# Kernel tuning notes

Measured on AMD Instinct MI355X. Metric: run time of the kernel, lower is better.

## Reference

```python
import jax, jax.numpy as jnp
import numpy as np

DIM = 2048
NH = 16
HD = DIM // NH  # 128


def setup_inputs() -> dict:
    key = jax.random.key(0)
    ks = jax.random.split(key, 9)
    s_in = 1.0 / np.sqrt(DIM)
    inp = {
        "x": jax.random.normal(ks[0], (2, 2048, DIM), dtype=jnp.float32),
        # torch Linear weights stored as (out, in); we keep (in, out) for x @ W
        "wq": jax.random.uniform(ks[1], (DIM, DIM), jnp.float32, -s_in, s_in),
        "bq": jax.random.uniform(ks[2], (DIM,), jnp.float32, -s_in, s_in),
        "wk": jax.random.uniform(ks[3], (DIM, HD), jnp.float32, -s_in, s_in),
        "bk": jax.random.uniform(ks[4], (HD,), jnp.float32, -s_in, s_in),
        "wv": jax.random.uniform(ks[5], (DIM, HD), jnp.float32, -s_in, s_in),
        "bv": jax.random.uniform(ks[6], (HD,), jnp.float32, -s_in, s_in),
        "wo": jax.random.uniform(ks[7], (DIM, DIM), jnp.float32, -s_in, s_in),
        "bo": jax.random.uniform(ks[8], (DIM,), jnp.float32, -s_in, s_in),
    }
    return inp


def reference(x, wq, bq, wk, bk, wv, bv, wo, bo):
    bs, sl, dim = x.shape
    q = x @ wq + bq                      # [b, s, dim]
    k = x @ wk + bk                      # [b, s, hd] (single shared KV head)
    v = x @ wv + bv                      # [b, s, hd]
    q = q.reshape(bs, sl, NH, HD)        # [b, s, h, hd]
    scale = 1.0 / np.sqrt(HD).astype(np.float32)
    # scores: broadcast single KV head over all query heads
    attn = jnp.einsum('bshd,btd->bhst', q, k) * scale   # [b, h, s, s]
    att = jax.nn.softmax(attn, axis=-1)
    o = jnp.einsum('bhst,btd->bshd', att, v)            # [b, s, h, hd]
    o = o.reshape(bs, sl, dim)
    return o @ wo + bo
```

## Files before the change

kernel.cpp:

```cpp
#include <hip/hip_runtime.h>
#include <hip/hip_bf16.h>
#include <math.h>

#define DIM 2048
#define NH 16
#define HD 128
#define BATCH 2
#define SEQ 2048
#define TOKENS (BATCH * SEQ)
#define NQKV (DIM + 2 * HD)

typedef __attribute__((ext_vector_type(8))) _Float16 f16x8;
typedef __attribute__((ext_vector_type(4))) float f32x4;
typedef unsigned short u16;
typedef unsigned int u32;

typedef union { u32 d[4]; f16x8 v; } frag_u;

__device__ __forceinline__ u16 f2h(float f) {
    union { _Float16 h; u16 u; } v; v.h = (_Float16)f; return v.u;
}
__device__ __forceinline__ void gll16(const void* g, void* l) {
    __builtin_amdgcn_global_load_lds(
        (const __attribute__((address_space(1))) unsigned int*)g,
        (__attribute__((address_space(3))) unsigned int*)l, 16, 0, 0);
}

__global__ __launch_bounds__(256) void conv_f16(
    const float* __restrict__ in, u16* __restrict__ out)
{
    const int i = blockIdx.x * 256 + threadIdx.x;
    const float4 v = ((const float4*)in)[i];
    ushort4 h;
    h.x = f2h(v.x); h.y = f2h(v.y); h.z = f2h(v.z); h.w = f2h(v.w);
    ((ushort4*)out)[i] = h;
}

__global__ __launch_bounds__(256) void transpose_f16(
    const float* __restrict__ W, u16* __restrict__ T, int K, int N, int rowoff)
{
    __shared__ float tile[32][33];
    const int k0 = blockIdx.x * 32;
    const int n0 = blockIdx.y * 32;
    const int tid = threadIdx.x;
#pragma unroll
    for (int i = 0; i < 4; ++i) {
        const int idx = tid + i * 256;
        const int r = idx >> 5, c = idx & 31;
        tile[r][c] = W[(size_t)(k0 + r) * N + n0 + c];
    }
    __syncthreads();
#pragma unroll
    for (int i = 0; i < 4; ++i) {
        const int idx = tid + i * 256;
        const int r = idx >> 5, c = idx & 31;
        T[(size_t)(rowoff + n0 + r) * K + k0 + c] = f2h(tile[c][r]);
    }
}

__global__ __launch_bounds__(256) void concat_bias(
    const float* __restrict__ bq, const float* __restrict__ bk,
    const float* __restrict__ bv, float* __restrict__ bc)
{
    const int i = blockIdx.x * 256 + threadIdx.x;
    float v;
    if (i < DIM) v = bq[i];
    else if (i < DIM + HD) v = bk[i - DIM];
    else v = bv[i - DIM - HD];
    bc[i] = v;
}

template <int MODE>
__global__ __launch_bounds__(256) void gemm_f16(
    const u16* __restrict__ A, const u16* __restrict__ B,
    const float* __restrict__ bias, float* __restrict__ Cf,
    u16* __restrict__ qdst, u16* __restrict__ kdst, u16* __restrict__ vtdst,
    float scale)
{
    constexpr int BK = 32;
    __shared__ u16 lds[2][2 * 128 * BK];

    const int tid = threadIdx.x;
    const int wid = tid >> 6;
    const int lane = tid & 63;
    const int lr = lane & 15;
    const int lhi = lane >> 4;
    const int wr = wid >> 1, wc = wid & 1;
    const int bm = blockIdx.y * 128;
    const int bn = blockIdx.x * 128;

    f32x4 acc[4][4];
#pragma unroll
    for (int i = 0; i < 4; ++i)
#pragma unroll
        for (int j = 0; j < 4; ++j) acc[i][j] = (f32x4){0.f, 0.f, 0.f, 0.f};

#define STAGE(buf_, k0_)                                                      \
    {                                                                         \
        _Pragma("unroll")                                                     \
        for (int rr = 0; rr < 2; ++rr) {                                      \
            const int slot = rr * 256 + tid;                                  \
            const int row = slot >> 2;                                        \
            const int gch = ((slot & 3) ^ ((row >> 1) & 3)) * 8;              \
            char* lbase = (char*)lds[buf_] + (size_t)(rr * 256 + wid * 64) * 16; \
            gll16(A + (size_t)(bm + row) * DIM + (k0_) + gch, lbase);         \
            gll16(B + (size_t)(bn + row) * DIM + (k0_) + gch, lbase + 8192);  \
        }                                                                     \
    }

    STAGE(0, 0);
    __syncthreads();

    int cur = 0;
    for (int k0 = 0; k0 < DIM; k0 += BK) {
        if (k0 + BK < DIM) STAGE(cur ^ 1, k0 + BK);

        f16x8 a[4], b[4];
#pragma unroll
        for (int i = 0; i < 4; ++i) {
            const int mrow = wr * 64 + i * 16 + lr;
            const int nrow = wc * 64 + i * 16 + lr;
            a[i] = *(const f16x8*)&lds[cur][mrow * BK + ((lhi ^ ((mrow >> 1) & 3)) * 8)];
            b[i] = *(const f16x8*)&lds[cur][4096 + nrow * BK + ((lhi ^ ((nrow >> 1) & 3)) * 8)];
        }
        __builtin_amdgcn_s_setprio(1);
#pragma unroll
        for (int i = 0; i < 4; ++i)
#pragma unroll
            for (int j = 0; j < 4; ++j)
                acc[i][j] = __builtin_amdgcn_mfma_f32_16x16x32_f16(a[i], b[j], acc[i][j], 0, 0, 0);
        __builtin_amdgcn_s_setprio(0);
        __syncthreads();
        cur ^= 1;
    }
#undef STAGE

    const float alpha = (MODE == 0 && bn < DIM) ? scale : 1.0f;
    float bj[4];
#pragma unroll
    for (int j = 0; j < 4; ++j) bj[j] = bias[bn + wc * 64 + j * 16 + lr];

#pragma unroll
    for (int i = 0; i < 4; ++i) {
#pragma unroll
        for (int j = 0; j < 4; ++j) {
#pragma unroll
            for (int r = 0; r < 4; ++r) {
                const int row = bm + wr * 64 + i * 16 + lhi * 4 + r;
                const int col = bn + wc * 64 + j * 16 + lr;
                const float val = (acc[i][j][r] + bj[j]) * alpha;
                if (MODE == 1) {
                    Cf[(size_t)row * DIM + col] = val;
                } else if (bn < DIM) {
                    qdst[(size_t)row * DIM + col] = f2h(val);
                } else if (bn < DIM + HD) {
                    kdst[(size_t)row * HD + (col - DIM)] = f2h(val);
                } else {
                    vtdst[(size_t)(col - DIM - HD) * TOKENS + row] = f2h(val);
                }
            }
        }
    }
}

__global__ __launch_bounds__(512, 4) void mqa_attn_f16(
    const u16* __restrict__ Q, const u16* __restrict__ Kg,
    const u16* __restrict__ Vtg, u16* __restrict__ Oh)
{
    __shared__ __align__(16) u16 smem[32768];

    const int tid = threadIdx.x;
    const int wid = tid >> 6;
    const int lane = tid & 63;
    const int lr = lane & 15;
    const int lhi = lane >> 4;
    const bool l5 = (lhi & 2) != 0;
    const int qg = wid & 3;
    const int half = wid >> 2;

    const int qt = blockIdx.x;
    const int h  = blockIdx.y;
    const int b  = blockIdx.z;
    const size_t bseq = (size_t)b * SEQ;
    const int q0 = qt * 128 + qg * 32;
    const int kvoff = half * 1024;

#define KS(hh, bb, r, c) smem[((hh) * 2 + (bb)) * 4096 + (r) * 128 + \
                              ((((c) >> 3) ^ ((r) & 7)) << 3)]
#define VS(hh, bb, d, c) smem[16384 + ((hh) * 2 + (bb)) * 4096 + (d) * 32 + \
                              (((((c) >> 3) & 3) ^ ((d) & 3)) << 3)]

    f16x8 qf[2][4];
#pragma unroll
    for (int mt = 0; mt < 2; ++mt) {
        const u16* qrow = Q + (bseq + q0 + mt * 16 + lr) * DIM + (size_t)h * HD;
#pragma unroll
        for (int kk = 0; kk < 4; ++kk)
            qf[mt][kk] = *(const f16x8*)(qrow + kk * 32 + lhi * 8);
    }

    f16x8 ones;
#pragma unroll
    for (int j = 0; j < 8; ++j) ones[j] = (_Float16)1.0f;

    f32x4 o[2][8];
#pragma unroll
    for (int mt = 0; mt < 2; ++mt)
#pragma unroll
        for (int dt = 0; dt < 8; ++dt) o[mt][dt] = (f32x4){0.f, 0.f, 0.f, 0.f};
    float m[2]    = {-INFINITY, -INFINITY};
    float lsum[2] = {0.f, 0.f};

#define STAGE_KV(buf_, t_)                                                    \
    {                                                                         \
        const int Ls = wid * 64 + lane;                                       \
        const int krow = Ls >> 4;                                             \
        const int kc = (Ls & 15) ^ (krow & 7);                                \
        const int vrow = Ls >> 2;                                             \
        const int vg = (Ls & 3) ^ (vrow & 3);                                 \
        _Pragma("unroll")                                                     \
        for (int i = 0; i < 2; ++i) {                                         \
            char* kb = (char*)smem + (size_t)((i * 2 + (buf_)) * 4096 + wid * 512) * 2; \
            char* vb = (char*)smem + (size_t)(16384 + (i * 2 + (buf_)) * 4096 + wid * 512) * 2; \
            const int kv0 = i * 1024 + (t_) * 32;                             \
            gll16(&Kg[(bseq + kv0 + krow) * HD + kc * 8], kb);                \
            gll16(&Vtg[(size_t)vrow * TOKENS + bseq + kv0 + vg * 8], vb);     \
        }                                                                     \
    }

    STAGE_KV(0, 0);
    __syncthreads();

    int cur = 0;
    for (int t = 0; t < 32; ++t) {
        if (t + 1 < 32) STAGE_KV(cur ^ 1, t + 1);

        f32x4 sc[2][2];
#pragma unroll
        for (int mt = 0; mt < 2; ++mt)
#pragma unroll
            for (int ct = 0; ct < 2; ++ct) sc[mt][ct] = (f32x4){0.f, 0.f, 0.f, 0.f};
        __builtin_amdgcn_s_setprio(1);
#pragma unroll
        for (int kk = 0; kk < 4; ++kk)
#pragma unroll
            for (int ct = 0; ct < 2; ++ct) {
                const f16x8 kf = *(const f16x8*)&KS(half, cur, ct * 16 + lr, kk * 32 + lhi * 8);
                sc[0][ct] = __builtin_amdgcn_mfma_f32_16x16x32_f16(kf, qf[0][kk], sc[0][ct], 0, 0, 0);
                sc[1][ct] = __builtin_amdgcn_mfma_f32_16x16x32_f16(kf, qf[1][kk], sc[1][ct], 0, 0, 0);
            }
        __builtin_amdgcn_s_setprio(0);

        frag_u pa[2];
        float al[2];
        bool anyg[2];
#pragma unroll
        for (int mt = 0; mt < 2; ++mt) {
            float pm = fmaxf(fmaxf(fmaxf(sc[mt][0][0], sc[mt][0][1]),
                                   fmaxf(sc[mt][0][2], sc[mt][0][3])),
                             fmaxf(fmaxf(sc[mt][1][0], sc[mt][1][1]),
                                   fmaxf(sc[mt][1][2], sc[mt][1][3])));
            pm = fmaxf(pm, __shfl_xor(pm, 16));
            pm = fmaxf(pm, __shfl_xor(pm, 32));

            const bool grow = pm > m[mt] + 8.f;
            const float mnew = grow ? pm : m[mt];
            al[mt] = grow ? __expf(m[mt] - mnew) : 1.f;
            anyg[mt] = __any(grow);
            m[mt] = mnew;

            u32 pk[2][2];
#pragma unroll
            for (int ct = 0; ct < 2; ++ct) {
                const float p0 = __expf(sc[mt][ct][0] - mnew);
                const float p1 = __expf(sc[mt][ct][1] - mnew);
                const float p2 = __expf(sc[mt][ct][2] - mnew);
                const float p3 = __expf(sc[mt][ct][3] - mnew);
                pk[ct][0] = __builtin_bit_cast(u32, __builtin_amdgcn_cvt_pkrtz(p0, p1));
                pk[ct][1] = __builtin_bit_cast(u32, __builtin_amdgcn_cvt_pkrtz(p2, p3));
            }
#pragma unroll
            for (int p = 0; p < 2; ++p) {
                const u32 X = pk[0][p];
                const u32 Y = pk[1][p];
                const u32 sx = __shfl_xor(X, 32);
                const u32 sy = __shfl_xor(Y, 32);
                const u32 X1 = l5 ? sy : X;
                const u32 Y1 = l5 ? Y : sx;
                const auto u2 = __builtin_amdgcn_permlane16_swap(X1, Y1, false, false);
                pa[mt].d[p]     = u2[0];
                pa[mt].d[2 + p] = u2[1];
            }

            if (anyg[mt]) {
#pragma unroll
                for (int dt = 0; dt < 8; ++dt)
#pragma unroll
                    for (int r = 0; r < 4; ++r)
                        o[mt][dt][r] *= al[mt];
                lsum[mt] *= al[mt];
            }
        }

        f32x4 lacc[2];
        lacc[0] = (f32x4){0.f, 0.f, 0.f, 0.f};
        lacc[1] = (f32x4){0.f, 0.f, 0.f, 0.f};
        __builtin_amdgcn_s_setprio(1);
        lacc[0] = __builtin_amdgcn_mfma_f32_16x16x32_f16(ones, pa[0].v, lacc[0], 0, 0, 0);
        lacc[1] = __builtin_amdgcn_mfma_f32_16x16x32_f16(ones, pa[1].v, lacc[1], 0, 0, 0);
#pragma unroll
        for (int dt = 0; dt < 8; ++dt) {
            const f16x8 vf = *(const f16x8*)&VS(half, cur, dt * 16 + lr, lhi * 8);
            o[0][dt] = __builtin_amdgcn_mfma_f32_16x16x32_f16(vf, pa[0].v, o[0][dt], 0, 0, 0);
            o[1][dt] = __builtin_amdgcn_mfma_f32_16x16x32_f16(vf, pa[1].v, o[1][dt], 0, 0, 0);
        }
        __builtin_amdgcn_s_setprio(0);
        lsum[0] += lacc[0][0];
        lsum[1] += lacc[1][0];

        __syncthreads();
        cur ^= 1;
    }
#undef STAGE_KV
#undef KS
#undef VS

    float* fs = (float*)smem;
#pragma unroll
    for (int mt = 0; mt < 2; ++mt) {
        __syncthreads();
        if (half == 1) {
#pragma unroll
            for (int dt = 0; dt < 8; ++dt)
#pragma unroll
                for (int r = 0; r < 4; ++r)
                    fs[qg * 2048 + (dt * 4 + r) * 64 + lane] = o[mt][dt][r];
            if (lhi == 0) {
                fs[8192 + qg * 16 + lr] = m[mt];
                fs[8192 + 64 + qg * 16 + lr] = lsum[mt];
            }
        }
        __syncthreads();
        if (half == 0) {
            const float m1 = fs[8192 + qg * 16 + lr];
            const float l1 = fs[8192 + 64 + qg * 16 + lr];
            const float mm = fmaxf(m[mt], m1);
            const float a0 = __expf(m[mt] - mm);
            const float a1 = __expf(m1 - mm);
            const float inv = 1.f / (lsum[mt] * a0 + l1 * a1);
            const size_t base = (bseq + q0 + mt * 16 + lr) * DIM + (size_t)h * HD + lhi * 4;
#pragma unroll
            for (int dt = 0; dt < 8; ++dt) {
                ushort4 h4;
#pragma unroll
                for (int r = 0; r < 4; ++r) {
                    const float o1 = fs[qg * 2048 + (dt * 4 + r) * 64 + lane];
                    const float val = (o[mt][dt][r] * a0 + o1 * a1) * inv;
                    ((u16*)&h4)[r] = f2h(val);
                }
                *(ushort4*)&Oh[base + dt * 16] = h4;
            }
        }
    }
}

extern "C" void kernel_launch(void* const* d_in, const int* in_sizes, int n_in,
                              void* d_out, int out_size, void* d_ws, size_t ws_size,
                              hipStream_t stream) {
    const float* x  = (const float*)d_in[0];
    const float* wq = (const float*)d_in[1];
    const float* bq = (const float*)d_in[2];
    const float* wk = (const float*)d_in[3];
    const float* bk = (const float*)d_in[4];
    const float* wv = (const float*)d_in[5];
    const float* bv = (const float*)d_in[6];
    const float* wo = (const float*)d_in[7];
    const float* bo = (const float*)d_in[8];
    float* out = (float*)d_out;

    char* w = (char*)d_ws;
    u16* xh     = (u16*)w;                 w += (size_t)TOKENS * DIM * 2;
    u16* wcat   = (u16*)w;                 w += (size_t)NQKV * DIM * 2;
    u16* woT    = (u16*)w;                 w += (size_t)DIM * DIM * 2;
    u16* qb     = (u16*)w;                 w += (size_t)TOKENS * DIM * 2;
    u16* kb     = (u16*)w;                 w += (size_t)TOKENS * HD * 2;
    u16* vtb    = (u16*)w;                 w += (size_t)TOKENS * HD * 2;
    float* bc   = (float*)w;               w += 16384;
    u16* Oh = xh;

    const float scale = 0.08838834764831845f;
    const dim3 blk(256);

    conv_f16<<<TOKENS * DIM / 4 / 256, blk, 0, stream>>>(x, xh);
    transpose_f16<<<dim3(DIM / 32, DIM / 32), blk, 0, stream>>>(wq, wcat, DIM, DIM, 0);
    transpose_f16<<<dim3(DIM / 32, HD / 32), blk, 0, stream>>>(wk, wcat, DIM, HD, DIM);
    transpose_f16<<<dim3(DIM / 32, HD / 32), blk, 0, stream>>>(wv, wcat, DIM, HD, DIM + HD);
    transpose_f16<<<dim3(DIM / 32, DIM / 32), blk, 0, stream>>>(wo, woT, DIM, DIM, 0);
    concat_bias<<<NQKV / 256, blk, 0, stream>>>(bq, bk, bv, bc);

    gemm_f16<0><<<dim3(NQKV / 128, TOKENS / 128), blk, 0, stream>>>(
        xh, wcat, bc, nullptr, qb, kb, vtb, scale);

    mqa_attn_f16<<<dim3(SEQ / 128, NH, BATCH), dim3(512), 0, stream>>>(qb, kb, vtb, Oh);

    gemm_f16<1><<<dim3(DIM / 128, TOKENS / 128), blk, 0, stream>>>(
        Oh, woT, bo, out, nullptr, nullptr, nullptr, 1.0f);
}
```

Before: 248.9 us.

## Split attention KV halves across blocks and merge partials in a separate kernel

The attention kernel previously ran 512-thread blocks in which two wave groups each handled half the KV sequence and merged through shared memory. Each block now has 256 threads and handles one KV half, with the half index carried in grid z. That doubles the block count and halves shared memory per block, which should improve occupancy and scheduling flexibility. Unnormalized partial outputs (fp16) plus the max and sum values are written to global workspace, and a new merge kernel combines them. The cost is an extra launch, extra global traffic for the partials, and an added fp16 rounding of the unnormalized partial outputs.

Result: slower. 265.5 us (+6.6%).

```diff
diff --git a/kernel.cpp b/kernel.cpp
--- a/kernel.cpp
+++ b/kernel.cpp
@@ -19,6 +19,9 @@
 
 __device__ __forceinline__ u16 f2h(float f) {
     union { _Float16 h; u16 u; } v; v.h = (_Float16)f; return v.u;
+}
+__device__ __forceinline__ float h2f(u16 u) {
+    union { u16 u; _Float16 h; } v; v.u = u; return (float)v.h;
 }
 __device__ __forceinline__ void gll16(const void* g, void* l) {
     __builtin_amdgcn_global_load_lds(
@@ -163,11 +166,13 @@
     }
 }
 
-__global__ __launch_bounds__(512, 4) void mqa_attn_f16(
+__global__ __launch_bounds__(256, 4) void mqa_attn_f16(
     const u16* __restrict__ Q, const u16* __restrict__ Kg,
-    const u16* __restrict__ Vtg, u16* __restrict__ Oh)
-{
-    __shared__ __align__(16) u16 smem[32768];
+    const u16* __restrict__ Vtg, u16* __restrict__ po,
+    float* __restrict__ pml, float* __restrict__ pll)
+{
+    __shared__ __align__(16) u16 Ks[2][32 * 128];
+    __shared__ __align__(16) u16 Vt[2][128 * 32];
 
     const int tid = threadIdx.x;
     const int wid = tid >> 6;
@@ -175,20 +180,18 @@
     const int lr = lane & 15;
     const int lhi = lane >> 4;
     const bool l5 = (lhi & 2) != 0;
-    const int qg = wid & 3;
-    const int half = wid >> 2;
 
     const int qt = blockIdx.x;
     const int h  = blockIdx.y;
-    const int b  = blockIdx.z;
+    const int zz = blockIdx.z;
+    const int b  = zz >> 1;
+    const int half = zz & 1;
     const size_t bseq = (size_t)b * SEQ;
-    const int q0 = qt * 128 + qg * 32;
+    const int q0 = qt * 128 + wid * 32;
     const int kvoff = half * 1024;
 
-#define KS(hh, bb, r, c) smem[((hh) * 2 + (bb)) * 4096 + (r) * 128 + \
-                              ((((c) >> 3) ^ ((r) & 7)) << 3)]
-#define VS(hh, bb, d, c) smem[16384 + ((hh) * 2 + (bb)) * 4096 + (d) * 32 + \
-                              (((((c) >> 3) & 3) ^ ((d) & 3)) << 3)]
+#define KS_AT(bb, r, c) Ks[bb][(r) * 128 + ((((c) >> 3) ^ ((r) & 7)) << 3)]
+#define VS_AT(bb, d, c) Vt[bb][(d) * 32 + (((((c) >> 3) & 3) ^ ((d) & 3)) << 3)]
 
     f16x8 qf[2][4];
 #pragma unroll
@@ -213,18 +216,18 @@
 
 #define STAGE_KV(buf_, t_)                                                    \
     {                                                                         \
-        const int Ls = wid * 64 + lane;                                       \
-        const int krow = Ls >> 4;                                             \
-        const int kc = (Ls & 15) ^ (krow & 7);                                \
-        const int vrow = Ls >> 2;                                             \
-        const int vg = (Ls & 3) ^ (vrow & 3);                                 \
         _Pragma("unroll")                                                     \
         for (int i = 0; i < 2; ++i) {                                         \
-            char* kb = (char*)smem + (size_t)((i * 2 + (buf_)) * 4096 + wid * 512) * 2; \
-            char* vb = (char*)smem + (size_t)(16384 + (i * 2 + (buf_)) * 4096 + wid * 512) * 2; \
-            const int kv0 = i * 1024 + (t_) * 32;                             \
-            gll16(&Kg[(bseq + kv0 + krow) * HD + kc * 8], kb);                \
-            gll16(&Vtg[(size_t)vrow * TOKENS + bseq + kv0 + vg * 8], vb);     \
+            const int L = i * 256 + tid;                                      \
+            char* kbase = (char*)&Ks[buf_][0] + (size_t)(i * 256 + wid * 64) * 16; \
+            char* vbase = (char*)&Vt[buf_][0] + (size_t)(i * 256 + wid * 64) * 16; \
+            const int krow = L >> 4;                                          \
+            const int kc = (L & 15) ^ (krow & 7);                             \
+            const int vrow = L >> 2;                                          \
+            const int vg = (L & 3) ^ (vrow & 3);                              \
+            const int kv0 = kvoff + (t_) * 32;                                \
+            gll16(&Kg[(bseq + kv0 + krow) * HD + kc * 8], kbase);             \
+            gll16(&Vtg[(size_t)vrow * TOKENS + bseq + kv0 + vg * 8], vbase);  \
         }                                                                     \
     }
 
@@ -245,15 +248,13 @@
         for (int kk = 0; kk < 4; ++kk)
 #pragma unroll
             for (int ct = 0; ct < 2; ++ct) {
-                const f16x8 kf = *(const f16x8*)&KS(half, cur, ct * 16 + lr, kk * 32 + lhi * 8);
+                const f16x8 kf = *(const f16x8*)&KS_AT(cur, ct * 16 + lr, kk * 32 + lhi * 8);
                 sc[0][ct] = __builtin_amdgcn_mfma_f32_16x16x32_f16(kf, qf[0][kk], sc[0][ct], 0, 0, 0);
                 sc[1][ct] = __builtin_amdgcn_mfma_f32_16x16x32_f16(kf, qf[1][kk], sc[1][ct], 0, 0, 0);
             }
         __builtin_amdgcn_s_setprio(0);
 
         frag_u pa[2];
-        float al[2];
-        bool anyg[2];
 #pragma unroll
         for (int mt = 0; mt < 2; ++mt) {
             float pm = fmaxf(fmaxf(fmaxf(sc[mt][0][0], sc[mt][0][1]),
@@ -265,8 +266,8 @@
 
             const bool grow = pm > m[mt] + 8.f;
             const float mnew = grow ? pm : m[mt];
-            al[mt] = grow ? __expf(m[mt] - mnew) : 1.f;
-            anyg[mt] = __any(grow);
+            const float al = grow ? __expf(m[mt] - mnew) : 1.f;
+            const bool anyg = __any(grow);
             m[mt] = mnew;
 
             u32 pk[2][2];
@@ -292,13 +293,13 @@
                 pa[mt].d[2 + p] = u2[1];
             }
 
-            if (anyg[mt]) {
+            if (anyg) {
 #pragma unroll
                 for (int dt = 0; dt < 8; ++dt)
 #pragma unroll
                     for (int r = 0; r < 4; ++r)
-                        o[mt][dt][r] *= al[mt];
-                lsum[mt] *= al[mt];
+                        o[mt][dt][r] *= al;
+                lsum[mt] *= al;
             }
         }
 
@@ -310,7 +311,7 @@
         lacc[1] = __builtin_amdgcn_mfma_f32_16x16x32_f16(ones, pa[1].v, lacc[1], 0, 0, 0);
 #pragma unroll
         for (int dt = 0; dt < 8; ++dt) {
-            const f16x8 vf = *(const f16x8*)&VS(half, cur, dt * 16 + lr, lhi * 8);
+            const f16x8 vf = *(const f16x8*)&VS_AT(cur, dt * 16 + lr, lhi * 8);
             o[0][dt] = __builtin_amdgcn_mfma_f32_16x16x32_f16(vf, pa[0].v, o[0][dt], 0, 0, 0);
             o[1][dt] = __builtin_amdgcn_mfma_f32_16x16x32_f16(vf, pa[1].v, o[1][dt], 0, 0, 0);
         }
@@ -322,46 +323,66 @@
         cur ^= 1;
     }
 #undef STAGE_KV
-#undef KS
-#undef VS
-
-    float* fs = (float*)smem;
+#undef KS_AT
+#undef VS_AT
+
+    u16* pob = po + (size_t)half * TOKENS * DIM;
 #pragma unroll
     for (int mt = 0; mt < 2; ++mt) {
-        __syncthreads();
-        if (half == 1) {
-#pragma unroll
-            for (int dt = 0; dt < 8; ++dt)
-#pragma unroll
-                for (int r = 0; r < 4; ++r)
-                    fs[qg * 2048 + (dt * 4 + r) * 64 + lane] = o[mt][dt][r];
-            if (lhi == 0) {
-                fs[8192 + qg * 16 + lr] = m[mt];
-                fs[8192 + 64 + qg * 16 + lr] = lsum[mt];
-            }
-        }
-        __syncthreads();
-        if (half == 0) {
-            const float m1 = fs[8192 + qg * 16 + lr];
-            const float l1 = fs[8192 + 64 + qg * 16 + lr];
-            const float mm = fmaxf(m[mt], m1);
-            const float a0 = __expf(m[mt] - mm);
-            const float a1 = __expf(m1 - mm);
-            const float inv = 1.f / (lsum[mt] * a0 + l1 * a1);
-            const size_t base = (bseq + q0 + mt * 16 + lr) * DIM + (size_t)h * HD + lhi * 4;
-#pragma unroll
-            for (int dt = 0; dt < 8; ++dt) {
-                ushort4 h4;
-#pragma unroll
-                for (int r = 0; r < 4; ++r) {
-                    const float o1 = fs[qg * 2048 + (dt * 4 + r) * 64 + lane];
-                    const float val = (o[mt][dt][r] * a0 + o1 * a1) * inv;
-                    ((u16*)&h4)[r] = f2h(val);
-                }
-                *(ushort4*)&Oh[base + dt * 16] = h4;
-            }
-        }
-    }
+        const int tok = (int)(bseq + q0 + mt * 16 + lr);
+        const size_t base = (size_t)tok * DIM + (size_t)h * HD + lhi * 4;
+#pragma unroll
+        for (int dt = 0; dt < 8; ++dt) {
+            ushort4 h4;
+            h4.x = f2h(o[mt][dt][0]);
+            h4.y = f2h(o[mt][dt][1]);
+            h4.z = f2h(o[mt][dt][2]);
+            h4.w = f2h(o[mt][dt][3]);
+            *(ushort4*)&pob[base + dt * 16] = h4;
+        }
+        if (lhi == 0) {
+            pml[(size_t)half * TOKENS * NH + (size_t)tok * NH + h] = m[mt];
+            pll[(size_t)half * TOKENS * NH + (size_t)tok * NH + h] = lsum[mt];
+        }
+    }
+}
+
+__global__ __launch_bounds__(256) void merge_halves(
+    const u16* __restrict__ po, const float* __restrict__ pml,
+    const float* __restrict__ pll, u16* __restrict__ Oh)
+{
+    const int idx = blockIdx.x * 256 + threadIdx.x;
+    const int token = idx >> 8;
+    const int rem = idx & 255;
+    const int h = rem >> 4;
+    const int d0 = (rem & 15) * 8;
+
+    const float m0 = pml[(size_t)token * NH + h];
+    const float l0 = pll[(size_t)token * NH + h];
+    const float m1 = pml[(size_t)TOKENS * NH + (size_t)token * NH + h];
+    const float l1 = pll[(size_t)TOKENS * NH + (size_t)token * NH + h];
+    const float mm = fmaxf(m0, m1);
+    const float a0 = __expf(m0 - mm);
+    const float a1 = __expf(m1 - mm);
+    const float inv = 1.f / (l0 * a0 + l1 * a1);
+
+    const size_t base = (size_t)token * DIM + (size_t)h * HD + d0;
+    const ushort4 o0a = *(const ushort4*)&po[base];
+    const ushort4 o0b = *(const ushort4*)&po[base + 4];
+    const ushort4 o1a = *(const ushort4*)&po[(size_t)TOKENS * DIM + base];
+    const ushort4 o1b = *(const ushort4*)&po[(size_t)TOKENS * DIM + base + 4];
+
+    ushort4 ra, rb;
+    ra.x = f2h((h2f(o0a.x) * a0 + h2f(o1a.x) * a1) * inv);
+    ra.y = f2h((h2f(o0a.y) * a0 + h2f(o1a.y) * a1) * inv);
+    ra.z = f2h((h2f(o0a.z) * a0 + h2f(o1a.z) * a1) * inv);
+    ra.w = f2h((h2f(o0a.w) * a0 + h2f(o1a.w) * a1) * inv);
+    rb.x = f2h((h2f(o0b.x) * a0 + h2f(o1b.x) * a1) * inv);
+    rb.y = f2h((h2f(o0b.y) * a0 + h2f(o1b.y) * a1) * inv);
+    rb.z = f2h((h2f(o0b.z) * a0 + h2f(o1b.z) * a1) * inv);
+    rb.w = f2h((h2f(o0b.w) * a0 + h2f(o1b.w) * a1) * inv);
+    *(ushort4*)&Oh[base] = ra;
+    *(ushort4*)&Oh[base + 4] = rb;
 }
 
 extern "C" void kernel_launch(void* const* d_in, const int* in_sizes, int n_in,
@@ -385,6 +406,9 @@
     u16* qb     = (u16*)w;                 w += (size_t)TOKENS * DIM * 2;
     u16* kb     = (u16*)w;                 w += (size_t)TOKENS * HD * 2;
     u16* vtb    = (u16*)w;                 w += (size_t)TOKENS * HD * 2;
+    u16* po     = (u16*)w;                 w += (size_t)2 * TOKENS * DIM * 2;
+    float* pml  = (float*)w;               w += (size_t)2 * TOKENS * NH * 4;
+    float* pll  = (float*)w;               w += (size_t)2 * TOKENS * NH * 4;
     float* bc   = (float*)w;               w += 16384;
     u16* Oh = xh;
 
@@ -401,7 +425,9 @@
     gemm_f16<0><<<dim3(NQKV / 128, TOKENS / 128), blk, 0, stream>>>(
         xh, wcat, bc, nullptr, qb, kb, vtb, scale);
 
-    mqa_attn_f16<<<dim3(SEQ / 128, NH, BATCH), dim3(512), 0, stream>>>(qb, kb, vtb, Oh);
+    mqa_attn_f16<<<dim3(SEQ / 128, NH, BATCH * 2), blk, 0, stream>>>(
+        qb, kb, vtb, po, pml, pll);
+    merge_halves<<<TOKENS * NH * 16 / 256, blk, 0, stream>>>(po, pml, pll, Oh);
 
     gemm_f16<1><<<dim3(DIM / 128, TOKENS / 128), blk, 0, stream>>>(
         Oh, woT, bo, out, nullptr, nullptr, nullptr, 1.0f);
```
